# Performance work log

Hardware: AMD Instinct MI355X
Metric: run time of the kernel (lower is better)

The kernel has to match this reference:

```python
import jax, jax.numpy as jnp
import numpy as np

B, NBAND, C, T = 2, 40, 64, 1500
NUM_CODE = 1024


def setup_inputs() -> dict:
    key = jax.random.key(0)
    k1, k2 = jax.random.split(key)
    x = jax.random.normal(k1, (B, NBAND, C, T), dtype=jnp.float32)
    # layer_idx == 0 init: unit-norm codes per band
    cb = jax.random.normal(k2, (NBAND, NUM_CODE, C), dtype=jnp.float32)
    eps = jnp.finfo(jnp.float32).eps
    cb = cb / jnp.sqrt(jnp.sum(cb * cb, axis=-1, keepdims=True) + eps)
    return {"x": x, "codebook": cb}


def reference(x, codebook):
    batch, nband, nchan, time = x.shape
    num_code = codebook.shape[1]
    # x.detach().permute(0,3,1,2).view(B*T, nband, nchan)
    xd = jax.lax.stop_gradient(x).transpose(0, 3, 1, 2).reshape(batch * time, nband, nchan)
    dist = (
        jnp.sum(xd * xd, axis=-1, keepdims=True)
        + jnp.sum(codebook * codebook, axis=-1)
        - 2.0 * jnp.einsum("nbc,bkc->nbk", xd, codebook)
    )
    min_idx = jnp.argmin(dist, axis=-1)  # [BT, nband]
    # per-band gather: quantized[n, b] = codebook[b, min_idx[n, b]]
    quantized = codebook[jnp.arange(nband)[None, :], min_idx]  # [BT, nband, nchan]
    # view(B, T, nband, nchan).permute(0,2,3,1)
    return quantized.reshape(batch, time, nband, nchan).transpose(0, 2, 3, 1)
```

## Files before the change

### kernel.cpp

```cpp
#include <hip/hip_runtime.h>


#define NBAND  40
#define CH     64
#define TT     1500
#define NCODE  1024
#define MT     128
#define PAD    68
#define THRESH 1e-3f

typedef short v8s __attribute__((ext_vector_type(8)));
typedef float v4f __attribute__((ext_vector_type(4)));

#define CBF_USHORTS ((size_t)NBAND * 32 * 8 * 64 * 8)
#define CBF_BYTES   (CBF_USHORTS * 2)
#define WS_NEEDED   (CBF_BYTES + (size_t)NBAND * NCODE * 4)

__device__ __forceinline__ unsigned short f2bf(float f) {
    unsigned u = __float_as_uint(f);
    return (unsigned short)((u + 0x7FFFu + ((u >> 16) & 1u)) >> 16);
}
__device__ __forceinline__ float bf2f(unsigned short h) {
    return __uint_as_float(((unsigned)h) << 16);
}
__device__ __forceinline__ unsigned ford(float f) {
    unsigned u = __float_as_uint(f);
    return (u & 0x80000000u) ? ~u : (u | 0x80000000u);
}
__device__ __forceinline__ unsigned long long packsk(float f, unsigned k) {
    return ((unsigned long long)ford(f) << 32) | (unsigned long long)k;
}

__global__ void vq_prep(const float* __restrict__ cb,
                        unsigned short* __restrict__ CBF,
                        float* __restrict__ C2) {
    const int g    = blockIdx.x;
    const int band = blockIdx.y;
    const int lane = threadIdx.x;
    const int col  = lane & 15;
    const int quad = lane >> 4;

    #pragma unroll
    for (int l = 0; l < 4; ++l) {
        const int ni = l >> 1, ks = l & 1;
        const int code = g * 32 + ni * 16 + col;
        const int c0   = ks * 32 + quad * 8;
        const float* src = cb + ((size_t)(band * NCODE + code)) * CH + c0;
        const float4 v0 = *(const float4*)src;
        const float4 v1 = *(const float4*)(src + 4);
        const float vv[8] = {v0.x, v0.y, v0.z, v0.w, v1.x, v1.y, v1.z, v1.w};
        union { unsigned short u[8]; v8s v; } hh, ll;
        #pragma unroll
        for (int j = 0; j < 8; ++j) {
            const unsigned short h = f2bf(vv[j]);
            hh.u[j] = h;
            ll.u[j] = f2bf(vv[j] - bf2f(h));
        }
        const size_t gb = (size_t)(band * 32 + g) * 8;
        *(v8s*)&CBF[(gb + l)     * 512 + lane * 8] = hh.v;
        *(v8s*)&CBF[(gb + 4 + l) * 512 + lane * 8] = ll.v;
    }
    if (lane < 32) {
        const int code = g * 32 + lane;
        const float* src = cb + ((size_t)(band * NCODE + code)) * CH;
        float s = 0.f;
        #pragma unroll 8
        for (int c = 0; c < CH; ++c) s = fmaf(src[c], src[c], s);
        C2[band * NCODE + code] = s;
    }
}

__global__ __launch_bounds__(256, 4)
void vq_main(const float* __restrict__ x,
             const float* __restrict__ cb,
             const unsigned short* __restrict__ CBF,
             const float* __restrict__ C2f,
             float* __restrict__ out) {
    __shared__ alignas(16) unsigned char SMEM[2 * MT * PAD * 2];
    __shared__ float c2_s[NCODE];
    __shared__ unsigned long long best_s[MT];
    __shared__ unsigned amb_s[4];
    __shared__ float xrow_s[CH];

    unsigned short* XH_s = (unsigned short*)SMEM;
    unsigned short* XL_s = XH_s + MT * PAD;

    const int tile  = blockIdx.x;
    const int band  = blockIdx.y;
    const int batch = blockIdx.z;
    const int t0    = tile * MT;

    const int tid  = threadIdx.x;
    const int wave = tid >> 6;
    const int lane = tid & 63;
    const int quad = lane >> 4;
    const int col  = lane & 15;

    if (tid < 4) amb_s[tid] = 0u;
    {
        const float* src = C2f + band * NCODE;
        #pragma unroll
        for (int i = 0; i < 4; ++i) c2_s[tid + 256 * i] = src[tid + 256 * i];
    }
    {
        const int c = tid & 63;
        const int g = tid >> 6;
        const float* src = x + ((size_t)(batch * NBAND + band) * CH + c) * TT + t0;
        #pragma unroll
        for (int i = 0; i < 8; ++i) {
            const int t = (g + 4 * i) * 4;
            float4 v = make_float4(0.f, 0.f, 0.f, 0.f);
            if (t0 + t + 3 < TT) v = *(const float4*)(src + t);
            const float vv[4] = {v.x, v.y, v.z, v.w};
            #pragma unroll
            for (int j = 0; j < 4; ++j) {
                const unsigned short h = f2bf(vv[j]);
                XH_s[(t + j) * PAD + c] = h;
                XL_s[(t + j) * PAD + c] = f2bf(vv[j] - bf2f(h));
            }
        }
    }
    __syncthreads();

    v8s ah[2][2], al[2][2];
    #pragma unroll
    for (int mi = 0; mi < 2; ++mi)
        #pragma unroll
        for (int ks = 0; ks < 2; ++ks) {
            const int off = (wave * 32 + mi * 16 + col) * PAD + ks * 32 + quad * 8;
            ah[mi][ks] = *(const v8s*)&XH_s[off];
            al[mi][ks] = *(const v8s*)&XL_s[off];
        }
    __syncthreads();

    float m1[8], m2[8];
    int   id8[8];
    #pragma unroll
    for (int i = 0; i < 8; ++i) { m1[i] = 3.4028235e38f; m2[i] = 3.4028235e38f; id8[i] = 0x7fffffff; }

    const unsigned short* fb = CBF + (size_t)(band * 32) * 8 * 512 + (size_t)lane * 8;

    for (int g = 0; g < 32; ++g) {
        const unsigned short* p = fb + (size_t)g * 8 * 512;
        v8s bh[2][2], bl[2][2];
        #pragma unroll
        for (int ni = 0; ni < 2; ++ni)
            #pragma unroll
            for (int ks = 0; ks < 2; ++ks) {
                bh[ni][ks] = *(const v8s*)(p + (ni * 2 + ks) * 512);
                bl[ni][ks] = *(const v8s*)(p + (4 + ni * 2 + ks) * 512);
            }
        v4f acc[2][2];
        #pragma unroll
        for (int mi = 0; mi < 2; ++mi)
            #pragma unroll
            for (int ni = 0; ni < 2; ++ni) acc[mi][ni] = (v4f){0.f, 0.f, 0.f, 0.f};
        #pragma unroll
        for (int ks = 0; ks < 2; ++ks) {
            #pragma unroll
            for (int mi = 0; mi < 2; ++mi)
                #pragma unroll
                for (int ni = 0; ni < 2; ++ni)
                    acc[mi][ni] = __builtin_amdgcn_mfma_f32_16x16x32_bf16(ah[mi][ks], bh[ni][ks], acc[mi][ni], 0, 0, 0);
            #pragma unroll
            for (int mi = 0; mi < 2; ++mi)
                #pragma unroll
                for (int ni = 0; ni < 2; ++ni)
                    acc[mi][ni] = __builtin_amdgcn_mfma_f32_16x16x32_bf16(ah[mi][ks], bl[ni][ks], acc[mi][ni], 0, 0, 0);
            #pragma unroll
            for (int mi = 0; mi < 2; ++mi)
                #pragma unroll
                for (int ni = 0; ni < 2; ++ni)
                    acc[mi][ni] = __builtin_amdgcn_mfma_f32_16x16x32_bf16(al[mi][ks], bh[ni][ks], acc[mi][ni], 0, 0, 0);
        }
        #pragma unroll
        for (int ni = 0; ni < 2; ++ni) {
            const float c2v = c2_s[g * 32 + ni * 16 + col];
            const int   kg  = g * 32 + ni * 16 + col;
            #pragma unroll
            for (int mi = 0; mi < 2; ++mi)
                #pragma unroll
                for (int r = 0; r < 4; ++r) {
                    const int j = mi * 4 + r;
                    const float s = fmaf(-2.f, acc[mi][ni][r], c2v);
                    m2[j] = fminf(m2[j], fmaxf(s, m1[j]));
                    const bool lt = s < m1[j];
                    m1[j]  = lt ? s : m1[j];
                    id8[j] = lt ? kg : id8[j];
                }
        }
    }
    __syncthreads();

    float* RM1 = (float*)SMEM;
    float* RM2 = RM1 + MT * 16;
    int*   RI  = (int*)(RM2 + MT * 16);
    #pragma unroll
    for (int j = 0; j < 8; ++j) {
        const int t = wave * 32 + (j >> 2) * 16 + quad * 4 + (j & 3);
        RM1[t * 16 + col] = m1[j];
        RM2[t * 16 + col] = m2[j];
        RI [t * 16 + col] = id8[j];
    }
    __syncthreads();

    if (tid < MT) {
        const int t = tid;
        float M1 = RM1[t * 16], M2 = RM2[t * 16];
        int   I  = RI[t * 16];
        #pragma unroll
        for (int j = 1; j < 16; ++j) {
            const float a1 = RM1[t * 16 + j];
            const float a2 = RM2[t * 16 + j];
            const int   ai = RI [t * 16 + j];
            if (a1 < M1 || (a1 == M1 && ai < I)) { M2 = fminf(M2, M1); M1 = a1; I = ai; }
            else                                  { M2 = fminf(M2, a1); }
            M2 = fminf(M2, a2);
        }
        best_s[t] = packsk(M1, (unsigned)I);
        if ((M2 - M1) <= THRESH && t0 + t < TT)
            atomicOr(&amb_s[t >> 5], 1u << (t & 31));
    }
    __syncthreads();

    for (int t = 0; t < MT; ++t) {
        if ((amb_s[t >> 5] >> (t & 31)) & 1u) {
            if (tid < CH) xrow_s[tid] = x[((size_t)(batch * NBAND + band) * CH + tid) * TT + t0 + t];
            if (tid == CH) best_s[t] = ~0ULL;
            __syncthreads();
            #pragma unroll
            for (int i = 0; i < 4; ++i) {
                const int k = tid * 4 + i;
                const float* crow = cb + ((size_t)(band * NCODE + k)) * CH;
                float dot = 0.f, c2e = 0.f;
                #pragma unroll 8
                for (int c = 0; c < CH; ++c) {
                    const float cv = crow[c];
                    dot = fmaf(cv, xrow_s[c], dot);
                    c2e = fmaf(cv, cv, c2e);
                }
                atomicMin(&best_s[t], packsk(fmaf(-2.f, dot, c2e), (unsigned)k));
            }
            __syncthreads();
        }
    }
    __syncthreads();

    {
        const int tloc  = tid & 127;
        const int chalf = tid >> 7;
        if (t0 + tloc < TT) {
            const unsigned idx = (unsigned)(best_s[tloc] & 0xFFFFFFFFull) & (NCODE - 1);
            const float* crow = cb + ((size_t)(band * NCODE + idx)) * CH;
            float* ob = out + ((size_t)(batch * NBAND + band) * CH) * TT + t0 + tloc;
            #pragma unroll
            for (int i = 0; i < 32; ++i) {
                const int c = chalf * 32 + i;
                ob[(size_t)c * TT] = crow[c];
            }
        }
    }
}

#define TN 128
#define KC 128
__global__ __launch_bounds__(256, 2)
void vq_fp32_kernel(const float* __restrict__ x,
                    const float* __restrict__ cb,
                    float* __restrict__ out) {
    __shared__ float XT_s[CH * TN];
    __shared__ float CBT_s[CH * KC];
    __shared__ float c2part[256];
    const int tile = blockIdx.x, band = blockIdx.y, batch = blockIdx.z;
    const int t0 = tile * TN;
    const int tid = threadIdx.x;
    const int tx = tid & 15, ty = tid >> 4;
    {
        const int c = tid >> 2, q = tid & 3;
        const float* src = x + ((size_t)(batch * NBAND + band) * CH + c) * TT + t0;
        #pragma unroll
        for (int i = 0; i < 8; ++i) {
            const int t = q * 32 + i * 4;
            float4 v = make_float4(0.f, 0.f, 0.f, 0.f);
            if (t0 + t < TT) v = *(const float4*)(src + t);
            *(float4*)&XT_s[c * TN + t] = v;
        }
    }
    float vmin[8]; int vidx[8];
    #pragma unroll
    for (int i = 0; i < 8; ++i) { vmin[i] = 3.4e38f; vidx[i] = 0x7fffffff; }
    for (int kc = 0; kc < NCODE; kc += KC) {
        __syncthreads();
        {
            const int k = tid >> 1, ch0 = (tid & 1) * 32;
            const float* src = cb + ((size_t)(band * NCODE + kc + k)) * CH + ch0;
            float s = 0.f;
            #pragma unroll
            for (int i = 0; i < 8; ++i) {
                const float4 v = *(const float4*)(src + i * 4);
                const int c0 = ch0 + i * 4;
                CBT_s[(c0 + 0) * KC + k] = v.x; CBT_s[(c0 + 1) * KC + k] = v.y;
                CBT_s[(c0 + 2) * KC + k] = v.z; CBT_s[(c0 + 3) * KC + k] = v.w;
                s = fmaf(v.x, v.x, s); s = fmaf(v.y, v.y, s);
                s = fmaf(v.z, v.z, s); s = fmaf(v.w, v.w, s);
            }
            c2part[tid] = s;
        }
        __syncthreads();
        float acc[8][8];
        #pragma unroll
        for (int ii = 0; ii < 8; ++ii)
            #pragma unroll
            for (int jj = 0; jj < 8; ++jj) acc[ii][jj] = 0.f;
        #pragma unroll 4
        for (int c = 0; c < CH; ++c) {
            const float4 xa0 = *(const float4*)&XT_s[c * TN + tx * 4];
            const float4 xa1 = *(const float4*)&XT_s[c * TN + 64 + tx * 4];
            const float4 cv0 = *(const float4*)&CBT_s[c * KC + ty * 4];
            const float4 cv1 = *(const float4*)&CBT_s[c * KC + 64 + ty * 4];
            const float xa[8] = {xa0.x, xa0.y, xa0.z, xa0.w, xa1.x, xa1.y, xa1.z, xa1.w};
            const float cv[8] = {cv0.x, cv0.y, cv0.z, cv0.w, cv1.x, cv1.y, cv1.z, cv1.w};
            #pragma unroll
            for (int ii = 0; ii < 8; ++ii)
                #pragma unroll
                for (int jj = 0; jj < 8; ++jj) acc[ii][jj] = fmaf(xa[ii], cv[jj], acc[ii][jj]);
        }
        #pragma unroll
        for (int jj = 0; jj < 8; ++jj) {
            const int kl = (jj < 4) ? (ty * 4 + jj) : (64 + ty * 4 + (jj - 4));
            const float c2v = c2part[2 * kl] + c2part[2 * kl + 1];
            const int kglob = kc + kl;
            #pragma unroll
            for (int ii = 0; ii < 8; ++ii) {
                const float score = fmaf(-2.f, acc[ii][jj], c2v);
                if (score < vmin[ii]) { vmin[ii] = score; vidx[ii] = kglob; }
            }
        }
    }
    __syncthreads();
    float* redv = XT_s;
    int* redi = (int*)(XT_s + TN * 16);
    int* idxs = (int*)(XT_s + TN * 32);
    #pragma unroll
    for (int ii = 0; ii < 8; ++ii) {
        const int t = (ii < 4) ? (tx * 4 + ii) : (64 + tx * 4 + (ii - 4));
        redv[t * 16 + ty] = vmin[ii];
        redi[t * 16 + ty] = vidx[ii];
    }
    __syncthreads();
    if (tid < TN) {
        float bv = redv[tid * 16]; int bi = redi[tid * 16];
        #pragma unroll
        for (int j = 1; j < 16; ++j) {
            const float v = redv[tid * 16 + j]; const int id = redi[tid * 16 + j];
            if (v < bv || (v == bv && id < bi)) { bv = v; bi = id; }
        }
        idxs[tid] = bi;
    }
    __syncthreads();
    {
        const int tloc = tid & 127, chalf = tid >> 7;
        if (t0 + tloc < TT) {
            const int idx = idxs[tloc];
            const float* crow = cb + ((size_t)(band * NCODE + idx)) * CH;
            float* ob = out + ((size_t)(batch * NBAND + band) * CH) * TT + t0 + tloc;
            #pragma unroll
            for (int i = 0; i < 32; ++i) {
                const int c = chalf * 32 + i;
                ob[(size_t)c * TT] = crow[c];
            }
        }
    }
}

extern "C" void kernel_launch(void* const* d_in, const int* in_sizes, int n_in,
                              void* d_out, int out_size, void* d_ws, size_t ws_size,
                              hipStream_t stream) {
    const float* x  = (const float*)d_in[0];
    const float* cb = (const float*)d_in[1];
    float* out = (float*)d_out;
    dim3 grid((TT + MT - 1) / MT, NBAND, 2);
    if (ws_size >= WS_NEEDED) {
        unsigned short* CBF = (unsigned short*)d_ws;
        float* C2 = (float*)((char*)d_ws + CBF_BYTES);
        vq_prep<<<dim3(32, NBAND), dim3(64), 0, stream>>>(cb, CBF, C2);
        vq_main<<<grid, dim3(256), 0, stream>>>(x, cb, CBF, C2, out);
    } else {
        vq_fp32_kernel<<<grid, dim3(256), 0, stream>>>(x, cb, out);
    }
}
```

Baseline: 218.7 us.

## Stage codebook groups into LDS via async double-buffered loads; fuse prep norms

The main loop now streams each 32-code codebook group from global memory into a double-buffered LDS region with global_load_lds, cooperatively split across the four waves. Each wave then reads its B fragments from LDS instead of every wave loading the same fragments straight from global memory. This cuts redundant global traffic and overlaps the next group's load with the current MFMA work, at the cost of a __syncthreads per group iteration. The prep kernel now uses 256-thread blocks and computes code squared norms from the values it already loaded, reduced with lane shuffles, instead of a separate serial per-code loop.

```diff
diff --git a/kernel.cpp b/kernel.cpp
--- a/kernel.cpp
+++ b/kernel.cpp
@@ -31,15 +31,23 @@
     return ((unsigned long long)ford(f) << 32) | (unsigned long long)k;
 }
 
-__global__ void vq_prep(const float* __restrict__ cb,
-                        unsigned short* __restrict__ CBF,
-                        float* __restrict__ C2) {
-    const int g    = blockIdx.x;
+typedef __attribute__((address_space(1))) const unsigned char* gas_p;
+typedef __attribute__((address_space(3))) unsigned char*       las_p;
+__device__ __forceinline__ void async_ld16(const void* g, void* l) {
+    __builtin_amdgcn_global_load_lds((gas_p)g, (las_p)l, 16, 0, 0);
+}
+
+__global__ __launch_bounds__(256)
+void vq_prep(const float* __restrict__ cb,
+             unsigned short* __restrict__ CBF,
+             float* __restrict__ C2) {
     const int band = blockIdx.y;
-    const int lane = threadIdx.x;
+    const int g    = blockIdx.x * 4 + (threadIdx.x >> 6);
+    const int lane = threadIdx.x & 63;
     const int col  = lane & 15;
     const int quad = lane >> 4;
 
+    float sq[2] = {0.f, 0.f};
     #pragma unroll
     for (int l = 0; l < 4; ++l) {
         const int ni = l >> 1, ks = l & 1;
@@ -55,18 +63,20 @@
             const unsigned short h = f2bf(vv[j]);
             hh.u[j] = h;
             ll.u[j] = f2bf(vv[j] - bf2f(h));
+            sq[ni] = fmaf(vv[j], vv[j], sq[ni]);
         }
         const size_t gb = (size_t)(band * 32 + g) * 8;
         *(v8s*)&CBF[(gb + l)     * 512 + lane * 8] = hh.v;
         *(v8s*)&CBF[(gb + 4 + l) * 512 + lane * 8] = ll.v;
     }
-    if (lane < 32) {
-        const int code = g * 32 + lane;
-        const float* src = cb + ((size_t)(band * NCODE + code)) * CH;
-        float s = 0.f;
-        #pragma unroll 8
-        for (int c = 0; c < CH; ++c) s = fmaf(src[c], src[c], s);
-        C2[band * NCODE + code] = s;
+    #pragma unroll
+    for (int ni = 0; ni < 2; ++ni) {
+        sq[ni] += __shfl_xor(sq[ni], 16);
+        sq[ni] += __shfl_xor(sq[ni], 32);
+    }
+    if (quad == 0) {
+        C2[band * NCODE + g * 32 + col]      = sq[0];
+        C2[band * NCODE + g * 32 + 16 + col] = sq[1];
     }
 }
 
@@ -76,7 +86,7 @@
              const unsigned short* __restrict__ CBF,
              const float* __restrict__ C2f,
              float* __restrict__ out) {
-    __shared__ alignas(16) unsigned char SMEM[2 * MT * PAD * 2];
+    __shared__ alignas(16) unsigned char SMEM[MT * PAD * 2 * 2];
     __shared__ float c2_s[NCODE];
     __shared__ unsigned long long best_s[MT];
     __shared__ unsigned amb_s[4];
@@ -138,40 +148,52 @@
     #pragma unroll
     for (int i = 0; i < 8; ++i) { m1[i] = 3.4028235e38f; m2[i] = 3.4028235e38f; id8[i] = 0x7fffffff; }
 
-    const unsigned short* fb = CBF + (size_t)(band * 32) * 8 * 512 + (size_t)lane * 8;
+    const unsigned short* fbase = CBF + (size_t)(band * 32) * 4096 + (size_t)lane * 8;
+    unsigned short* LBUF = (unsigned short*)SMEM;
+
+    auto stage_group = [&](int g, int buf) {
+        #pragma unroll
+        for (int i = 0; i < 2; ++i) {
+            const int p = wave * 2 + i;
+            async_ld16(fbase + (size_t)g * 4096 + p * 512,
+                       LBUF + (size_t)buf * 4096 + p * 512);
+        }
+    };
+
+    stage_group(0, 0);
 
     for (int g = 0; g < 32; ++g) {
-        const unsigned short* p = fb + (size_t)g * 8 * 512;
-        v8s bh[2][2], bl[2][2];
-        #pragma unroll
-        for (int ni = 0; ni < 2; ++ni)
-            #pragma unroll
-            for (int ks = 0; ks < 2; ++ks) {
-                bh[ni][ks] = *(const v8s*)(p + (ni * 2 + ks) * 512);
-                bl[ni][ks] = *(const v8s*)(p + (4 + ni * 2 + ks) * 512);
-            }
+        __syncthreads();
+        if (g + 1 < 32) stage_group(g + 1, (g + 1) & 1);
+
+        const unsigned short* lb = LBUF + (size_t)(g & 1) * 4096 + lane * 8;
         v4f acc[2][2];
         #pragma unroll
         for (int mi = 0; mi < 2; ++mi)
             #pragma unroll
             for (int ni = 0; ni < 2; ++ni) acc[mi][ni] = (v4f){0.f, 0.f, 0.f, 0.f};
+
         #pragma unroll
         for (int ks = 0; ks < 2; ++ks) {
-            #pragma unroll
-            for (int mi = 0; mi < 2; ++mi)
-                #pragma unroll
-                for (int ni = 0; ni < 2; ++ni)
-                    acc[mi][ni] = __builtin_amdgcn_mfma_f32_16x16x32_bf16(ah[mi][ks], bh[ni][ks], acc[mi][ni], 0, 0, 0);
-            #pragma unroll
-            for (int mi = 0; mi < 2; ++mi)
-                #pragma unroll
-                for (int ni = 0; ni < 2; ++ni)
-                    acc[mi][ni] = __builtin_amdgcn_mfma_f32_16x16x32_bf16(ah[mi][ks], bl[ni][ks], acc[mi][ni], 0, 0, 0);
-            #pragma unroll
-            for (int mi = 0; mi < 2; ++mi)
-                #pragma unroll
-                for (int ni = 0; ni < 2; ++ni)
-                    acc[mi][ni] = __builtin_amdgcn_mfma_f32_16x16x32_bf16(al[mi][ks], bh[ni][ks], acc[mi][ni], 0, 0, 0);
+            const v8s bh0 = *(const v8s*)(lb + (0 * 2 + ks) * 512);
+            const v8s bh1 = *(const v8s*)(lb + (1 * 2 + ks) * 512);
+            const v8s bl0 = *(const v8s*)(lb + (4 + 0 * 2 + ks) * 512);
+            const v8s bl1 = *(const v8s*)(lb + (4 + 1 * 2 + ks) * 512);
+            #pragma unroll
+            for (int mi = 0; mi < 2; ++mi) {
+                acc[mi][0] = __builtin_amdgcn_mfma_f32_16x16x32_bf16(ah[mi][ks], bh0, acc[mi][0], 0, 0, 0);
+                acc[mi][1] = __builtin_amdgcn_mfma_f32_16x16x32_bf16(ah[mi][ks], bh1, acc[mi][1], 0, 0, 0);
+            }
+            #pragma unroll
+            for (int mi = 0; mi < 2; ++mi) {
+                acc[mi][0] = __builtin_amdgcn_mfma_f32_16x16x32_bf16(ah[mi][ks], bl0, acc[mi][0], 0, 0, 0);
+                acc[mi][1] = __builtin_amdgcn_mfma_f32_16x16x32_bf16(ah[mi][ks], bl1, acc[mi][1], 0, 0, 0);
+            }
+            #pragma unroll
+            for (int mi = 0; mi < 2; ++mi) {
+                acc[mi][0] = __builtin_amdgcn_mfma_f32_16x16x32_bf16(al[mi][ks], bh0, acc[mi][0], 0, 0, 0);
+                acc[mi][1] = __builtin_amdgcn_mfma_f32_16x16x32_bf16(al[mi][ks], bh1, acc[mi][1], 0, 0, 0);
+            }
         }
         #pragma unroll
         for (int ni = 0; ni < 2; ++ni) {
@@ -383,7 +405,7 @@
     if (ws_size >= WS_NEEDED) {
         unsigned short* CBF = (unsigned short*)d_ws;
         float* C2 = (float*)((char*)d_ws + CBF_BYTES);
-        vq_prep<<<dim3(32, NBAND), dim3(64), 0, stream>>>(cb, CBF, C2);
+        vq_prep<<<dim3(8, NBAND), dim3(256), 0, stream>>>(cb, CBF, C2);
         vq_main<<<grid, dim3(256), 0, stream>>>(x, cb, CBF, C2, out);
     } else {
         vq_fp32_kernel<<<grid, dim3(256), 0, stream>>>(x, cb, out);
```

Result: no change. 215.3 us (-1.6%).
